# Kernel tuning notes

Hardware: AMD Instinct MI355X
Metric: run time of the kernel (lower is better)

Reference implementation:

```python
import jax, jax.numpy as jnp
import numpy as np

DIM = 1024
H = 16
HD = DIM // H


def setup_inputs() -> dict:
    key = jax.random.key(0)
    ks = jax.random.split(key, 14)
    B, L1, L2 = 8, 512, 512
    s = 0.02
    return {
        "seq1": jax.random.normal(ks[0], (B, L1, DIM), jnp.float32),
        "seq2": jax.random.normal(ks[1], (B, L2, DIM), jnp.float32),
        "atc1": jax.random.normal(ks[2], (B, L1, 5), jnp.float32),
        "atc2": jax.random.normal(ks[3], (B, L2, 5), jnp.float32),
        "Wq": jax.random.normal(ks[4], (DIM, DIM), jnp.float32) * s,
        "bq": jnp.zeros((DIM,), jnp.float32),
        "Wk": jax.random.normal(ks[5], (DIM, DIM), jnp.float32) * s,
        "bk": jnp.zeros((DIM,), jnp.float32),
        "Wv": jax.random.normal(ks[6], (DIM, DIM), jnp.float32) * s,
        "bv": jnp.zeros((DIM,), jnp.float32),
        "Wo": jax.random.normal(ks[7], (DIM, DIM), jnp.float32) * s,
        "bo": jnp.zeros((DIM,), jnp.float32),
        "U": jax.random.normal(ks[8], (H, 5, 5), jnp.float32) * 0.02,
        "mix_param": jnp.float32(0.0),
    }


def reference(seq1, seq2, atc1, atc2, Wq, bq, Wk, bk, Wv, bv, Wo, bo, U, mix_param):
    B, L1, _ = seq1.shape
    L2 = seq2.shape[1]
    # projections; weights stored (out,in) like nn.Linear -> x @ W.T + b
    q = (seq1 @ Wq.T + bq).reshape(B, L1, H, HD).transpose(0, 2, 1, 3)  # b h l1 d
    k = (seq2 @ Wk.T + bk).reshape(B, L2, H, HD).transpose(0, 2, 1, 3)
    v = (seq2 @ Wv.T + bv).reshape(B, L2, H, HD).transpose(0, 2, 1, 3)
    std_scores = jnp.einsum('bhid,bhjd->bhij', q, k) / jnp.sqrt(jnp.float32(HD))
    # per-head Atchley bias: bip, hpq, bjq -> bhij (vectorized over heads)
    bio_scores = jnp.einsum('bip,hpq,bjq->bhij', atc1, U, atc2)
    mix = jnp.tanh(mix_param)
    mix_ratio = (mix + 1.0) / 2.0
    attn = (1.0 - mix_ratio) * jax.nn.softmax(std_scores, axis=-1) \
         + mix_ratio * jax.nn.softmax(bio_scores, axis=-1)
    out = jnp.einsum('bhij,bhjd->bhid', attn, v)  # b h l1 d
    out = out.transpose(0, 2, 1, 3).reshape(B, L1, DIM)
    return out @ Wo.T + bo
```

## Files before the change

kernel.cpp:

```cpp
#include <hip/hip_runtime.h>
#include <hip/hip_bf16.h>

typedef __attribute__((ext_vector_type(8))) short short8;
typedef __attribute__((ext_vector_type(8))) unsigned short ushort8;
typedef __attribute__((ext_vector_type(4))) float f32x4;
typedef unsigned short u16;

#define DIM 1024
#define NH 16
#define HD 64
#define NB 8
#define L 512
#define ML (NB * L)

__device__ __forceinline__ u16 f2bf(float f) {
  union { float f; unsigned int u; } x; x.f = f;
  unsigned int r = x.u + 0x7FFFu + ((x.u >> 16) & 1u);
  return (u16)(r >> 16);
}

__device__ __forceinline__ unsigned int pkbf(float a, float b) {
  union { __hip_bfloat162 h; unsigned int u; } r;
  r.h = __float22bfloat162_rn(float2{a, b});
  return r.u;
}

__device__ __forceinline__ void gld16(u16* lds, const u16* g) {
  __builtin_amdgcn_global_load_lds(
      (__attribute__((address_space(1))) void*)g,
      (__attribute__((address_space(3))) void*)lds, 16, 0, 0);
}

__global__ __launch_bounds__(256) void cvt_all(
    const float* __restrict__ s1, const float* __restrict__ s2,
    const float* __restrict__ wq, const float* __restrict__ wk,
    const float* __restrict__ wv, const float* __restrict__ wo,
    u16* __restrict__ o1, u16* __restrict__ o2, u16* __restrict__ oq,
    u16* __restrict__ ok, u16* __restrict__ ov, u16* __restrict__ oo) {
  const int blk = blockIdx.x;
  const float* src; u16* dst; int rel;
  if (blk < 2048)       { src = s1; dst = o1; rel = blk; }
  else if (blk < 4096)  { src = s2; dst = o2; rel = blk - 2048; }
  else if (blk < 4608)  { src = wq; dst = oq; rel = blk - 4096; }
  else if (blk < 5120)  { src = wk; dst = ok; rel = blk - 4608; }
  else if (blk < 5632)  { src = wv; dst = ov; rel = blk - 5120; }
  else                  { src = wo; dst = oo; rel = blk - 5632; }
  const int i = rel * 256 + threadIdx.x;
  const float4 v0 = reinterpret_cast<const float4*>(src)[2 * i];
  const float4 v1 = reinterpret_cast<const float4*>(src)[2 * i + 1];
  ushort8 o;
  o[0] = f2bf(v0.x); o[1] = f2bf(v0.y); o[2] = f2bf(v0.z); o[3] = f2bf(v0.w);
  o[4] = f2bf(v1.x); o[5] = f2bf(v1.y); o[6] = f2bf(v1.z); o[7] = f2bf(v1.w);
  reinterpret_cast<ushort8*>(dst)[i] = o;
}

template <int BN, bool OUT_F32, bool KV, int NT>
__global__ __launch_bounds__(256) void gemm_db(
    const u16* __restrict__ A, const u16* __restrict__ Bw,
    const float* __restrict__ b0, const float* __restrict__ b1,
    void* __restrict__ Cp, int N, int K) {
  __shared__ __align__(16) u16 As[2][128 * 32];
  __shared__ __align__(16) u16 Bs[2][BN * 32];
  const int tid = threadIdx.x;
  const int lane = tid & 63;
  const int w = tid >> 6;
  const int ll = lane & 15, lg = lane >> 4;
  const int wm = (w >> 1) * 64;
  const int wn = (w & 1) * (BN / 2);
  constexpr int NF = BN / 32;
  const int bid = blockIdx.x;
  const int tile = (bid & 7) * (gridDim.x >> 3) + (bid >> 3);
  const int bm = (tile / NT) * 128;
  const int bn = (tile % NT) * BN;

  f32x4 acc[4][NF];
#pragma unroll
  for (int m = 0; m < 4; ++m)
#pragma unroll
    for (int n = 0; n < NF; ++n) acc[m][n] = (f32x4){0.f, 0.f, 0.f, 0.f};

  auto stage = [&](int bi, int kt) {
#pragma unroll
    for (int it = 0; it < 2; ++it) {
      const int slot = it * 256 + tid;
      gld16(&As[bi][(it * 256 + w * 64) * 8],
            A + (size_t)(bm + (slot >> 2)) * K + kt + (slot & 3) * 8);
    }
#pragma unroll
    for (int it = 0; it < BN / 64; ++it) {
      const int slot = it * 256 + tid;
      gld16(&Bs[bi][(it * 256 + w * 64) * 8],
            Bw + (size_t)(bn + (slot >> 2)) * K + kt + (slot & 3) * 8);
    }
  };

  stage(0, 0);
  __syncthreads();
  int cur = 0;
  for (int kt = 0; kt < K; kt += 32) {
    if (kt + 32 < K) stage(cur ^ 1, kt + 32);
    short8 af[4], bf[NF];
#pragma unroll
    for (int m = 0; m < 4; ++m)
      af[m] = *reinterpret_cast<const short8*>(&As[cur][(wm + m * 16 + ll) * 32 + lg * 8]);
#pragma unroll
    for (int n = 0; n < NF; ++n)
      bf[n] = *reinterpret_cast<const short8*>(&Bs[cur][(wn + n * 16 + ll) * 32 + lg * 8]);
#pragma unroll
    for (int m = 0; m < 4; ++m)
#pragma unroll
      for (int n = 0; n < NF; ++n)
        acc[m][n] = __builtin_amdgcn_mfma_f32_16x16x32_bf16(af[m], bf[n], acc[m][n], 0, 0, 0);
    __syncthreads();
    cur ^= 1;
  }

#pragma unroll
  for (int m = 0; m < 4; ++m) {
#pragma unroll
    for (int n = 0; n < NF; ++n) {
#pragma unroll
      for (int r = 0; r < 4; ++r) {
        const int row = bm + wm + m * 16 + lg * 4 + r;
        const int col = bn + wn + n * 16 + ll;
        float bb;
        if constexpr (KV) bb = (col < DIM) ? b0[col] : b1[col - DIM];
        else bb = b0[col];
        const float v = acc[m][n][r] + bb;
        if constexpr (OUT_F32)
          reinterpret_cast<float*>(Cp)[(size_t)row * N + col] = v;
        else
          reinterpret_cast<u16*>(Cp)[(size_t)row * N + col] = f2bf(v);
      }
    }
  }
}

__global__ __launch_bounds__(256) void transpose_v(const u16* __restrict__ kvb,
                                                   u16* __restrict__ vt) {
  __shared__ u16 T[64][65];
  const int jt = blockIdx.x, h = blockIdx.y, bb = blockIdx.z;
  const int tid = threadIdx.x;
#pragma unroll
  for (int rep = 0; rep < 16; ++rep) {
    const int idx = rep * 256 + tid;
    const int jr = idx >> 6, d = idx & 63;
    T[jr][d] = kvb[(size_t)(bb * L + jt * 64 + jr) * 2048 + DIM + h * HD + d];
  }
  __syncthreads();
#pragma unroll
  for (int rep = 0; rep < 16; ++rep) {
    const int idx = rep * 256 + tid;
    const int dr = idx >> 6, j = idx & 63;
    vt[(size_t)((bb * NH + h) * HD + dr) * L + jt * 64 + j] = T[j][dr];
  }
}

__global__ __launch_bounds__(256) void a1u_kernel(const float* __restrict__ atc1,
                                                  const float* __restrict__ U,
                                                  float* __restrict__ a1u) {
  const int idx = blockIdx.x * 256 + threadIdx.x;
  if (idx >= NB * NH * L * 5) return;
  const int q = idx % 5;
  const int i = (idx / 5) & (L - 1);
  const int h = (idx / (5 * L)) & (NH - 1);
  const int b = idx / (5 * L * NH);
  float s = 0.f;
#pragma unroll
  for (int p = 0; p < 5; ++p)
    s += atc1[(size_t)(b * L + i) * 5 + p] * U[(h * 5 + p) * 5 + q];
  a1u[idx] = s;
}

__global__ __launch_bounds__(256, 4) void attn3(
    const u16* __restrict__ qb, const u16* __restrict__ kvb,
    const u16* __restrict__ vt, const float* __restrict__ a1u,
    const float* __restrict__ atc2, const float* __restrict__ mixp,
    u16* __restrict__ attb) {
  __shared__ __align__(16) float Sf[16 * 512];
  const int tid = threadIdx.x;
  const int wv = tid >> 6;
  const int lane = tid & 63;
  const int ll = lane & 15, lg = lane >> 4;
  const int bid = blockIdx.x;
  const int slot = bid >> 3;
  const int bh = (bid & 7) * 16 + (slot >> 5);
  const int it = slot & 31;
  const int b = bh >> 4, h = bh & 15;
  const int i0 = it * 16;

  const float ratio = (tanhf(mixp[0]) + 1.0f) * 0.5f;

  const u16* qp = qb + (size_t)(b * L + i0 + ll) * DIM + h * HD + lg * 8;
  const short8 aq0 = *reinterpret_cast<const short8*>(qp);
  const short8 aq1 = *reinterpret_cast<const short8*>(qp + 32);

  float bs[4][8];
  {
    float r2a[20], r2b[20];
    {
      const float4* pa = reinterpret_cast<const float4*>(atc2 + ((size_t)b * L + 4 * lane) * 5);
      const float4* pb = reinterpret_cast<const float4*>(atc2 + ((size_t)b * L + 256 + 4 * lane) * 5);
#pragma unroll
      for (int u = 0; u < 5; ++u) {
        const float4 ta = pa[u], tb = pb[u];
        r2a[4 * u] = ta.x; r2a[4 * u + 1] = ta.y; r2a[4 * u + 2] = ta.z; r2a[4 * u + 3] = ta.w;
        r2b[4 * u] = tb.x; r2b[4 * u + 1] = tb.y; r2b[4 * u + 2] = tb.z; r2b[4 * u + 3] = tb.w;
      }
    }
    const float* a1p = a1u + ((size_t)(b * NH + h) * L + i0 + wv * 4) * 5;
    float a1v[20];
#pragma unroll
    for (int p = 0; p < 20; ++p) a1v[p] = a1p[p];
#pragma unroll
    for (int ri = 0; ri < 4; ++ri) {
#pragma unroll
      for (int j = 0; j < 4; ++j) {
        float sa = 0.f, sb = 0.f;
#pragma unroll
        for (int p = 0; p < 5; ++p) {
          sa += a1v[ri * 5 + p] * r2a[j * 5 + p];
          sb += a1v[ri * 5 + p] * r2b[j * 5 + p];
        }
        bs[ri][j] = sa; bs[ri][j + 4] = sb;
      }
    }
  }

#pragma unroll
  for (int jt8 = 0; jt8 < 8; ++jt8) {
    const int jj = wv * 8 + jt8;
    const u16* kp = kvb + (size_t)(b * L + jj * 16 + ll) * 2048 + h * HD + lg * 8;
    const short8 k0 = *reinterpret_cast<const short8*>(kp);
    const short8 k1 = *reinterpret_cast<const short8*>(kp + 32);
    f32x4 s = (f32x4){0.f, 0.f, 0.f, 0.f};
    s = __builtin_amdgcn_mfma_f32_16x16x32_bf16(aq0, k0, s, 0, 0, 0);
    s = __builtin_amdgcn_mfma_f32_16x16x32_bf16(aq1, k1, s, 0, 0, 0);
    const int cfb = jj * 4 + (ll >> 2);
#pragma unroll
    for (int r = 0; r < 4; ++r) {
      const int row = lg * 4 + r;
      Sf[row * 512 + (((cfb ^ (row & 7)) << 2) | (ll & 3))] = s[r] * 0.125f;
    }
  }
  __syncthreads();

#pragma unroll
  for (int ri = 0; ri < 4; ++ri) {
    const int i = wv * 4 + ri;
    const int p1 = lane ^ (i & 7);
    const float4 x1 = *reinterpret_cast<const float4*>(&Sf[i * 512 + (p1 << 2)]);
    const float4 x2 = *reinterpret_cast<const float4*>(&Sf[i * 512 + ((64 + p1) << 2)]);
    float e1[8], e2[8];
    e1[0] = __expf(x1.x); e1[1] = __expf(x1.y); e1[2] = __expf(x1.z); e1[3] = __expf(x1.w);
    e1[4] = __expf(x2.x); e1[5] = __expf(x2.y); e1[6] = __expf(x2.z); e1[7] = __expf(x2.w);
#pragma unroll
    for (int j = 0; j < 8; ++j) e2[j] = __expf(bs[ri][j]);
    float l1 = 0.f, l2 = 0.f;
#pragma unroll
    for (int j = 0; j < 8; ++j) { l1 += e1[j]; l2 += e2[j]; }
#pragma unroll
    for (int off = 32; off > 0; off >>= 1) {
      l1 += __shfl_xor(l1, off);
      l2 += __shfl_xor(l2, off);
    }
    const float sc1 = (1.f - ratio) / l1, sc2 = ratio / l2;
    float p[8];
#pragma unroll
    for (int j = 0; j < 8; ++j) p[j] = sc1 * e1[j] + sc2 * e2[j];
    char* rowb = reinterpret_cast<char*>(Sf) + i * 2048;
    uint2 w0; w0.x = pkbf(p[0], p[1]); w0.y = pkbf(p[2], p[3]);
    uint2 w1; w1.x = pkbf(p[4], p[5]); w1.y = pkbf(p[6], p[7]);
    *reinterpret_cast<uint2*>(rowb + 8 * lane) = w0;
    *reinterpret_cast<uint2*>(rowb + 512 + 8 * lane) = w1;
  }
  __syncthreads();

  f32x4 O = (f32x4){0.f, 0.f, 0.f, 0.f};
  const u16* vbase = vt + ((size_t)(b * NH + h) * HD + wv * 16 + ll) * L;
  const char* Pb = reinterpret_cast<const char*>(Sf) + ll * 2048;
#pragma unroll
  for (int kk = 0; kk < 16; ++kk) {
    const short8 pa = *reinterpret_cast<const short8*>(Pb + kk * 64 + lg * 16);
    const short8 bv = *reinterpret_cast<const short8*>(vbase + kk * 32 + lg * 8);
    O = __builtin_amdgcn_mfma_f32_16x16x32_bf16(pa, bv, O, 0, 0, 0);
  }
#pragma unroll
  for (int r = 0; r < 4; ++r)
    attb[(size_t)(b * L + i0 + lg * 4 + r) * DIM + h * HD + wv * 16 + ll] = f2bf(O[r]);
}

extern "C" void kernel_launch(void* const* d_in, const int* in_sizes, int n_in,
                              void* d_out, int out_size, void* d_ws, size_t ws_size,
                              hipStream_t stream) {
  (void)in_sizes; (void)n_in; (void)out_size; (void)ws_size;
  const float* seq1 = (const float*)d_in[0];
  const float* seq2 = (const float*)d_in[1];
  const float* atc1 = (const float*)d_in[2];
  const float* atc2 = (const float*)d_in[3];
  const float* Wq = (const float*)d_in[4];
  const float* bq = (const float*)d_in[5];
  const float* Wk = (const float*)d_in[6];
  const float* bk = (const float*)d_in[7];
  const float* Wv = (const float*)d_in[8];
  const float* bv = (const float*)d_in[9];
  const float* Wo = (const float*)d_in[10];
  const float* bo = (const float*)d_in[11];
  const float* U = (const float*)d_in[12];
  const float* mixp = (const float*)d_in[13];

  char* ws = (char*)d_ws;
  const size_t SEQB = (size_t)ML * DIM * sizeof(u16);
  const size_t WB = (size_t)DIM * DIM * sizeof(u16);
  size_t o = 0;
  u16* s1b = (u16*)(ws + o); o += SEQB;
  u16* s2b = (u16*)(ws + o); o += SEQB;
  u16* wqb = (u16*)(ws + o); o += WB;
  u16* wkvb = (u16*)(ws + o); o += 2 * WB;
  u16* wob = (u16*)(ws + o); o += WB;
  u16* qb = (u16*)(ws + o); o += SEQB;
  u16* kvb = (u16*)(ws + o); o += 2 * SEQB;
  u16* vtb = (u16*)(ws + o); o += SEQB;
  u16* attb = (u16*)(ws + o); o += SEQB;
  float* a1u = (float*)(ws + o); o += (size_t)NB * NH * L * 5 * sizeof(float);

  cvt_all<<<6144, 256, 0, stream>>>(seq1, seq2, Wq, Wk, Wv, Wo, s1b, s2b, wqb,
                                    wkvb, wkvb + (size_t)DIM * DIM, wob);

  gemm_db<64, false, false, 16><<<512, 256, 0, stream>>>(s1b, wqb, bq, bq, qb, DIM, DIM);
  gemm_db<128, false, true, 16><<<512, 256, 0, stream>>>(s2b, wkvb, bk, bv, kvb, 2048, DIM);

  transpose_v<<<dim3(L / 64, NH, NB), 256, 0, stream>>>(kvb, vtb);
  a1u_kernel<<<(NB * NH * L * 5 + 255) / 256, 256, 0, stream>>>(atc1, U, a1u);

  attn3<<<4096, 256, 0, stream>>>(qb, kvb, vtb, a1u, atc2, mixp, attb);

  gemm_db<64, true, false, 16><<<512, 256, 0, stream>>>(attb, wob, bo, bo, (float*)d_out, DIM, DIM);
}
```

Measured before the change: 259.0 us.

## Widen GEMM K-tile to 64 with XOR-swizzled LDS and prefetch V in attention

The GEMM now stages 64-wide K slices and XOR-swizzles the 16-byte chunks in LDS, which halves the number of barriers per K loop and avoids bank conflicts on the fragment reads. The attention kernel issues the first half of the V loads before the softmax barrier and the second half during the P·V loop. It also swizzles the bf16 P layout in LDS to cut bank conflicts. The costs are twice the LDS per GEMM block and more registers in the attention kernel, which could lower occupancy.

```diff
diff --git a/kernel.cpp b/kernel.cpp
--- a/kernel.cpp
+++ b/kernel.cpp
@@ -59,8 +59,8 @@
     const u16* __restrict__ A, const u16* __restrict__ Bw,
     const float* __restrict__ b0, const float* __restrict__ b1,
     void* __restrict__ Cp, int N, int K) {
-  __shared__ __align__(16) u16 As[2][128 * 32];
-  __shared__ __align__(16) u16 Bs[2][BN * 32];
+  __shared__ __align__(16) u16 As[2][128 * 64];
+  __shared__ __align__(16) u16 Bs[2][BN * 64];
   const int tid = threadIdx.x;
   const int lane = tid & 63;
   const int w = tid >> 6;
@@ -81,36 +81,47 @@
 
   auto stage = [&](int bi, int kt) {
 #pragma unroll
-    for (int it = 0; it < 2; ++it) {
+    for (int it = 0; it < 4; ++it) {
       const int slot = it * 256 + tid;
+      const int row = slot >> 3, pch = slot & 7;
       gld16(&As[bi][(it * 256 + w * 64) * 8],
-            A + (size_t)(bm + (slot >> 2)) * K + kt + (slot & 3) * 8);
-    }
-#pragma unroll
-    for (int it = 0; it < BN / 64; ++it) {
+            A + (size_t)(bm + row) * K + kt + ((pch ^ (row & 7)) * 8));
+    }
+#pragma unroll
+    for (int it = 0; it < BN / 32; ++it) {
       const int slot = it * 256 + tid;
+      const int row = slot >> 3, pch = slot & 7;
       gld16(&Bs[bi][(it * 256 + w * 64) * 8],
-            Bw + (size_t)(bn + (slot >> 2)) * K + kt + (slot & 3) * 8);
+            Bw + (size_t)(bn + row) * K + kt + ((pch ^ (row & 7)) * 8));
     }
   };
 
   stage(0, 0);
   __syncthreads();
   int cur = 0;
-  for (int kt = 0; kt < K; kt += 32) {
-    if (kt + 32 < K) stage(cur ^ 1, kt + 32);
-    short8 af[4], bf[NF];
-#pragma unroll
-    for (int m = 0; m < 4; ++m)
-      af[m] = *reinterpret_cast<const short8*>(&As[cur][(wm + m * 16 + ll) * 32 + lg * 8]);
-#pragma unroll
-    for (int n = 0; n < NF; ++n)
-      bf[n] = *reinterpret_cast<const short8*>(&Bs[cur][(wn + n * 16 + ll) * 32 + lg * 8]);
-#pragma unroll
-    for (int m = 0; m < 4; ++m)
-#pragma unroll
-      for (int n = 0; n < NF; ++n)
-        acc[m][n] = __builtin_amdgcn_mfma_f32_16x16x32_bf16(af[m], bf[n], acc[m][n], 0, 0, 0);
+  for (int kt = 0; kt < K; kt += 64) {
+    if (kt + 64 < K) stage(cur ^ 1, kt + 64);
+#pragma unroll
+    for (int s = 0; s < 2; ++s) {
+      short8 af[4], bf[NF];
+#pragma unroll
+      for (int m = 0; m < 4; ++m) {
+        const int row = wm + m * 16 + ll;
+        af[m] = *reinterpret_cast<const short8*>(
+            &As[cur][row * 64 + (((s * 4 + lg) ^ (row & 7)) * 8)]);
+      }
+#pragma unroll
+      for (int n = 0; n < NF; ++n) {
+        const int row = wn + n * 16 + ll;
+        bf[n] = *reinterpret_cast<const short8*>(
+            &Bs[cur][row * 64 + (((s * 4 + lg) ^ (row & 7)) * 8)]);
+      }
+#pragma unroll
+      for (int m = 0; m < 4; ++m)
+#pragma unroll
+        for (int n = 0; n < NF; ++n)
+          acc[m][n] = __builtin_amdgcn_mfma_f32_16x16x32_bf16(af[m], bf[n], acc[m][n], 0, 0, 0);
+    }
     __syncthreads();
     cur ^= 1;
   }
@@ -172,7 +183,7 @@
   a1u[idx] = s;
 }
 
-__global__ __launch_bounds__(256, 4) void attn3(
+__global__ __launch_bounds__(256, 4) void attn4(
     const u16* __restrict__ qb, const u16* __restrict__ kvb,
     const u16* __restrict__ vt, const float* __restrict__ a1u,
     const float* __restrict__ atc2, const float* __restrict__ mixp,
@@ -243,6 +254,13 @@
       Sf[row * 512 + (((cfb ^ (row & 7)) << 2) | (ll & 3))] = s[r] * 0.125f;
     }
   }
+
+  const u16* vbase = vt + ((size_t)(b * NH + h) * HD + wv * 16 + ll) * L;
+  short8 va[8];
+#pragma unroll
+  for (int kk = 0; kk < 8; ++kk)
+    va[kk] = *reinterpret_cast<const short8*>(vbase + kk * 32 + lg * 8);
+
   __syncthreads();
 
 #pragma unroll
@@ -269,21 +287,29 @@
 #pragma unroll
     for (int j = 0; j < 8; ++j) p[j] = sc1 * e1[j] + sc2 * e2[j];
     char* rowb = reinterpret_cast<char*>(Sf) + i * 2048;
+    const int off0 = (((lane >> 1) ^ (i & 7)) << 4) | ((lane & 1) << 3);
     uint2 w0; w0.x = pkbf(p[0], p[1]); w0.y = pkbf(p[2], p[3]);
     uint2 w1; w1.x = pkbf(p[4], p[5]); w1.y = pkbf(p[6], p[7]);
-    *reinterpret_cast<uint2*>(rowb + 8 * lane) = w0;
-    *reinterpret_cast<uint2*>(rowb + 512 + 8 * lane) = w1;
+    *reinterpret_cast<uint2*>(rowb + off0) = w0;
+    *reinterpret_cast<uint2*>(rowb + 512 + off0) = w1;
   }
   __syncthreads();
 
   f32x4 O = (f32x4){0.f, 0.f, 0.f, 0.f};
-  const u16* vbase = vt + ((size_t)(b * NH + h) * HD + wv * 16 + ll) * L;
   const char* Pb = reinterpret_cast<const char*>(Sf) + ll * 2048;
-#pragma unroll
-  for (int kk = 0; kk < 16; ++kk) {
-    const short8 pa = *reinterpret_cast<const short8*>(Pb + kk * 64 + lg * 16);
-    const short8 bv = *reinterpret_cast<const short8*>(vbase + kk * 32 + lg * 8);
-    O = __builtin_amdgcn_mfma_f32_16x16x32_bf16(pa, bv, O, 0, 0, 0);
+  short8 vb[8];
+#pragma unroll
+  for (int kk = 0; kk < 8; ++kk) {
+    vb[kk] = *reinterpret_cast<const short8*>(vbase + (8 + kk) * 32 + lg * 8);
+    const short8 pa = *reinterpret_cast<const short8*>(
+        Pb + (((kk * 4 + lg) ^ (ll & 7)) << 4));
+    O = __builtin_amdgcn_mfma_f32_16x16x32_bf16(pa, va[kk], O, 0, 0, 0);
+  }
+#pragma unroll
+  for (int kk = 8; kk < 16; ++kk) {
+    const short8 pa = *reinterpret_cast<const short8*>(
+        Pb + (((kk * 4 + lg) ^ (ll & 7)) << 4));
+    O = __builtin_amdgcn_mfma_f32_16x16x32_bf16(pa, vb[kk - 8], O, 0, 0, 0);
   }
 #pragma unroll
   for (int r = 0; r < 4; ++r)
@@ -333,7 +359,7 @@
   transpose_v<<<dim3(L / 64, NH, NB), 256, 0, stream>>>(kvb, vtb);
   a1u_kernel<<<(NB * NH * L * 5 + 255) / 256, 256, 0, stream>>>(atc1, U, a1u);
 
-  attn3<<<4096, 256, 0, stream>>>(qb, kvb, vtb, a1u, atc2, mixp, attb);
+  attn4<<<4096, 256, 0, stream>>>(qb, kvb, vtb, a1u, atc2, mixp, attb);
 
   gemm_db<64, true, false, 16><<<512, 256, 0, stream>>>(attb, wob, bo, bo, (float*)d_out, DIM, DIM);
 }
```

New measurement: 258.1 us. About the same (-0.4%).
